# Optimization experiments

Measured on AMD Instinct MI355X. Metric: run time of the kernel, lower is better.

Reference implementation:

```python
import jax, jax.numpy as jnp
import numpy as np

T = 8192
INPUT = 1024
TRACE = 64
CTX = 16
OUT = 1024
EPS = 1e-5  # equinox LayerNorm default


def _linear(key, out_f, in_f):
    k1, k2 = jax.random.split(key)
    lim = 1.0 / np.sqrt(in_f)
    w = jax.random.uniform(k1, (out_f, in_f), minval=-lim, maxval=lim, dtype=jnp.float32)
    b = jax.random.uniform(k2, (out_f,), minval=-lim, maxval=lim, dtype=jnp.float32)
    return w, b


def setup_inputs() -> dict:
    key = jax.random.key(0)
    ks = jax.random.split(key, 8)
    x = jax.random.normal(ks[0], (T, INPUT), dtype=jnp.float32)
    start = jax.random.randint(ks[1], (T,), 0, 2).astype(bool)
    next_done = jax.random.randint(ks[2], (T,), 0, 2).astype(bool)
    state_re = jnp.zeros((1, TRACE, CTX), dtype=jnp.float32)
    state_im = jnp.zeros((1, TRACE, CTX), dtype=jnp.float32)
    pre_w, pre_b = _linear(ks[3], TRACE, INPUT)
    gi_w, gi_b = _linear(ks[4], TRACE, INPUT)
    go_w, go_b = _linear(ks[5], OUT, INPUT)
    skip_w, skip_b = _linear(ks[6], OUT, INPUT)
    mix_w, mix_b = _linear(ks[7], OUT, 2 * TRACE * CTX)
    # ffa.init: deterministic decay rates a and oscillation freqs b
    ffa_a = jnp.linspace(1e-6, 0.5, TRACE, dtype=jnp.float32)
    ffa_b = (2.0 * jnp.pi / jnp.exp(jnp.linspace(jnp.log(1.0), jnp.log(1024.0), CTX))).astype(jnp.float32)
    return dict(x=x, state_re=state_re, state_im=state_im, start=start, next_done=next_done,
                pre_w=pre_w, pre_b=pre_b, gi_w=gi_w, gi_b=gi_b, go_w=go_w, go_b=go_b,
                skip_w=skip_w, skip_b=skip_b, mix_w=mix_w, mix_b=mix_b,
                ffa_a=ffa_a, ffa_b=ffa_b)


def _ffa_apply(ffa_a, ffa_b, gated_x, state0, start):
    """Resettable complex linear recurrence: s_t = gamma * s_{t-1} + x_t, reset at episode starts.
    gamma = exp(-|a| + i b), outer over (trace, context). Parallelized with an associative scan
    over monoid elements (reset_flag, state, elapsed_steps)."""
    Tn, m = gated_x.shape
    c = ffa_b.shape[0]
    ab = jax.lax.complex(
        jnp.broadcast_to(-jnp.abs(ffa_a)[None, :, None], (1, m, c)),
        jnp.broadcast_to(ffa_b[None, None, :], (1, m, c)),
    )  # [1, m, c] complex: log-gamma per unit timestep

    xc = jnp.broadcast_to(gated_x[:, :, None].astype(jnp.complex64), (Tn, m, c))
    # prepend carried-in recurrent state: timestep 0, no reset
    x_e = jnp.concatenate([state0.astype(jnp.complex64), xc], axis=0)          # [T+1, m, c]
    s_e = jnp.concatenate([jnp.zeros((1, 1, 1), bool), start[:, None, None]], axis=0)
    i_e = jnp.concatenate([jnp.zeros((1, 1, 1), jnp.float32),
                           jnp.ones((Tn, 1, 1), jnp.float32)], axis=0)

    def op(a, b):
        s1, x1, i1 = a
        s2, x2, i2 = b
        # zero the carried state across episode boundaries
        x1 = jnp.where(s2, 0.0, x1)
        i1 = jnp.where(s2, 0.0, i1)
        g = jnp.exp(ab * i2.astype(jnp.complex64))  # decay over i2 elapsed steps
        return (jnp.logical_or(s1, s2), x1 * g + x2, i1 + i2)

    _, states, _ = jax.lax.associative_scan(op, (s_e, x_e, i_e), axis=0)
    return states[1:]  # [T, m, c] complex64


def reference(x, state_re, state_im, start, next_done,
              pre_w, pre_b, gi_w, gi_b, go_w, go_b,
              skip_w, skip_b, mix_w, mix_b, ffa_a, ffa_b):
    gate_in = jax.nn.sigmoid(x @ gi_w.T + gi_b)          # [T, trace]
    pre = x @ pre_w.T + pre_b                            # [T, trace]
    gated_x = pre * gate_in

    state0 = jax.lax.complex(state_re, state_im)         # [1, trace, ctx]
    state = _ffa_apply(ffa_a, ffa_b, gated_x, state0, start)  # [T, trace, ctx] complex

    z_in = jnp.concatenate([jnp.real(state), jnp.imag(state)], axis=-1)
    z_in = z_in.reshape(state.shape[0], -1)              # [T, 2*trace*ctx]
    z = z_in @ mix_w.T + mix_b                           # [T, out]

    gate_out = jax.nn.sigmoid(x @ go_w.T + go_b)         # [T, out]
    skip = x @ skip_w.T + skip_b                         # [T, out]

    zg = z * gate_out
    mu = zg.mean(-1, keepdims=True)
    var = ((zg - mu) ** 2).mean(-1, keepdims=True)
    ln = (zg - mu) / jnp.sqrt(var + EPS)                 # LayerNorm, no affine

    out = ln + skip * (1.0 - gate_out)
    final_state = state[-1:]
    return out, final_state


if __name__ == "__main__":
    inp = setup_inputs()
    out, fs = jax.jit(reference)(**inp)
    print(out.shape, out.dtype, fs.shape, fs.dtype)
```

## Files before the change

### kernel.cpp

```cpp
#include <hip/hip_runtime.h>
#include <math.h>

#define T_DIM 8192
#define IN_DIM 1024
#define TRACE 64
#define CTX 16
#define OUT_DIM 1024
#define KMIX 2048

typedef __attribute__((ext_vector_type(8))) short bf16x8;
typedef __attribute__((ext_vector_type(4))) float f32x4;
typedef __attribute__((ext_vector_type(16))) float f32x16;

__device__ __forceinline__ unsigned short f2bf(float f) {
    unsigned int u = __float_as_uint(f);
    u = (u + 0x7FFFu + ((u >> 16) & 1u)) >> 16;
    return (unsigned short)u;
}
__device__ __forceinline__ float bf2f(unsigned short b) {
    return __uint_as_float(((unsigned int)b) << 16);
}

__device__ __forceinline__ void gl2lds16(const void* g, void* l) {
    __builtin_amdgcn_global_load_lds(
        (const __attribute__((address_space(1))) unsigned int*)g,
        (__attribute__((address_space(3))) unsigned int*)l,
        16, 0, 0);
}


__global__ __launch_bounds__(256) void c0_conv(const float* __restrict__ x,
        const float* __restrict__ gw, const float* __restrict__ sw, const float* __restrict__ mw,
        const float* __restrict__ pw, const float* __restrict__ giw,
        const void* __restrict__ startp,
        unsigned short* __restrict__ xb, unsigned short* __restrict__ gob,
        unsigned short* __restrict__ skb, unsigned short* __restrict__ mixb,
        unsigned short* __restrict__ pwb, unsigned short* __restrict__ gwb,
        unsigned char* __restrict__ mask, unsigned long long* __restrict__ mask64)
{
    if (blockIdx.x == 0) {
        __shared__ int nonbool;
        int tid = threadIdx.x;
        if (tid == 0) nonbool = 0;
        __syncthreads();
        const unsigned int* wv = (const unsigned int*)startp;
        #pragma unroll
        for (int p = 0; p < 8; p++) {
            unsigned int a = wv[tid * 8 + p];
            if (a > 1u) nonbool = 1;
        }
        __syncthreads();
        if (nonbool) {
            const unsigned char* s8 = (const unsigned char*)startp;
            for (int i = tid; i < T_DIM; i += 256) mask[i] = (unsigned char)(s8[i] != 0);
        } else {
            const int* s32 = (const int*)startp;
            for (int i = tid; i < T_DIM; i += 256) mask[i] = (unsigned char)(s32[i] != 0);
        }
        __syncthreads();
        if (tid < 128) {
            unsigned long long wv2 = 0ull;
            int base = tid * 64;
            #pragma unroll 8
            for (int b2 = 0; b2 < 64; b2++)
                wv2 |= ((unsigned long long)(mask[base + b2] & 1)) << b2;
            mask64[tid] = wv2;
        }
    }
    const size_t QX = 2097152, QG = 262144, QS = 262144, QP = 16384, QI = 16384;
    const size_t totalA = QX + QG + QS + QP + QI;
    for (size_t q = (size_t)blockIdx.x * blockDim.x + threadIdx.x; q < totalA;
         q += (size_t)gridDim.x * blockDim.x) {
        const float* src; unsigned short* dst; size_t i;
        if (q < QX)               { src = x;   dst = xb;   i = q; }
        else if (q < QX+QG)       { src = gw;  dst = gob;  i = q - QX; }
        else if (q < QX+QG+QS)    { src = sw;  dst = skb;  i = q - QX - QG; }
        else if (q < QX+QG+QS+QP) { src = pw;  dst = pwb;  i = q - QX - QG - QS; }
        else                      { src = giw; dst = gwb;  i = q - QX - QG - QS - QP; }
        float4 v = *(const float4*)(src + i * 4);
        ushort4 o;
        o.x = f2bf(v.x); o.y = f2bf(v.y); o.z = f2bf(v.z); o.w = f2bf(v.w);
        *(ushort4*)(dst + i * 4) = o;
    }
    const size_t QM = 524288;
    for (size_t q = (size_t)blockIdx.x * blockDim.x + threadIdx.x; q < QM;
         q += (size_t)gridDim.x * blockDim.x) {
        float4 v = *(const float4*)(mw + q * 4);
        int flat = (int)(q * 4);
        int n  = flat >> 11;
        int kk = flat & 2047;
        int mm = kk >> 5;
        int w_ = kk & 31;
        int p  = w_ >> 4;
        int cc = w_ & 15;
        int kb = (n << 11) + mm * 32 + (cc << 1) + p;
        mixb[kb]     = f2bf(v.x);
        mixb[kb + 2] = f2bf(v.y);
        mixb[kb + 4] = f2bf(v.z);
        mixb[kb + 6] = f2bf(v.w);
    }
}

__global__ __launch_bounds__(256) void k1_mfma(const unsigned short* __restrict__ xb,
        const unsigned short* __restrict__ pwb, const unsigned short* __restrict__ gwb,
        const float* __restrict__ pre_b, const float* __restrict__ gi_b,
        float* __restrict__ gxT)
{
    __shared__ __align__(16) unsigned short As[1024];
    __shared__ __align__(16) unsigned short Bs[4096];
    __shared__ float sgE[64][33];

    const int tid = threadIdx.x;
    const int t0 = blockIdx.x * 32;
    const int lane = tid & 63, w = tid >> 6;
    const int quad = lane >> 4, l16 = lane & 15;
    const int r = tid >> 2, s4 = tid & 3;
    const int csw = (s4 - ((r >> 1) & 3)) & 3;

    f32x4 acc[2][2];
    const f32x4 zero4 = {0.f, 0.f, 0.f, 0.f};
    #pragma unroll
    for (int mi = 0; mi < 2; mi++)
        #pragma unroll
        for (int ni = 0; ni < 2; ni++) acc[mi][ni] = zero4;

    const int sfr = (quad + ((l16 >> 1) & 3)) & 3;

    for (int k0 = 0; k0 < IN_DIM; k0 += 32) {
        __syncthreads();
        if (tid < 128) {
            int ra = tid >> 2;
            int ca = ((tid & 3) - ((ra >> 1) & 3)) & 3;
            gl2lds16(xb + (size_t)(t0 + ra) * IN_DIM + k0 + ca * 8, As + tid * 8);
        }
        gl2lds16(pwb + (size_t)r * IN_DIM + k0 + csw * 8, Bs + tid * 8);
        gl2lds16(gwb + (size_t)r * IN_DIM + k0 + csw * 8, Bs + 2048 + tid * 8);
        asm volatile("s_waitcnt vmcnt(0)" ::: "memory");
        __syncthreads();
        bf16x8 af[2], bf[2];
        #pragma unroll
        for (int mi = 0; mi < 2; mi++)
            af[mi] = *(const bf16x8*)&As[(mi * 16 + l16) * 32 + sfr * 8];
        #pragma unroll
        for (int ni = 0; ni < 2; ni++)
            bf[ni] = *(const bf16x8*)&Bs[(w * 32 + ni * 16 + l16) * 32 + sfr * 8];
        #pragma unroll
        for (int mi = 0; mi < 2; mi++)
            #pragma unroll
            for (int ni = 0; ni < 2; ni++)
                acc[mi][ni] = __builtin_amdgcn_mfma_f32_16x16x32_bf16(af[mi], bf[ni], acc[mi][ni], 0, 0, 0);
    }

    if (w >= 2) {
        #pragma unroll
        for (int mi = 0; mi < 2; mi++)
            #pragma unroll
            for (int ni = 0; ni < 2; ni++) {
                int mg = (w - 2) * 32 + ni * 16 + l16;
                float gb = gi_b[mg];
                #pragma unroll
                for (int rr = 0; rr < 4; rr++) {
                    int tl = mi * 16 + quad * 4 + rr;
                    sgE[mg][tl] = 1.f / (1.f + expf(-(acc[mi][ni][rr] + gb)));
                }
            }
    }
    __syncthreads();
    if (w < 2) {
        #pragma unroll
        for (int mi = 0; mi < 2; mi++)
            #pragma unroll
            for (int ni = 0; ni < 2; ni++) {
                int mp = w * 32 + ni * 16 + l16;
                float pb = pre_b[mp];
                float4 o;
                float* po = &o.x;
                #pragma unroll
                for (int rr = 0; rr < 4; rr++) {
                    int tl = mi * 16 + quad * 4 + rr;
                    po[rr] = (acc[mi][ni][rr] + pb) * sgE[mp][tl];
                }
                *(float4*)&gxT[(size_t)mp * T_DIM + t0 + mi * 16 + quad * 4] = o;
            }
    }
}

__global__ __launch_bounds__(1024, 1) void k2_scan(const float* __restrict__ gxT,
        const unsigned long long* __restrict__ mask64,
        const float* __restrict__ state_re, const float* __restrict__ state_im,
        const float* __restrict__ ffa_a, const float* __restrict__ ffa_b,
        unsigned short* __restrict__ zinb, float* __restrict__ fstate)
{
    const int m = blockIdx.x;
    const int tid = threadIdx.x;
    const int c = tid & 15, j = tid >> 4;
    __shared__ __align__(16) float gxs[8192 + 128];
    __shared__ float Br[16][65], Bi[16][65], Er[16][65], Ei[16][65];
    __shared__ unsigned char Rf[16][65];

    const float am = -fabsf(ffa_a[m]);
    const float bc = ffa_b[c];
    const float er = expf(am);
    const float gr = er * cosf(bc);
    const float gi = er * sinf(bc);

    {
        const float4* gx4 = (const float4*)(gxT + (size_t)m * T_DIM);
        #pragma unroll
        for (int it = 0; it < 2; it++) {
            int g = it * 1024 + tid;
            float4 v = gx4[g];
            int t = g * 4;
            gxs[t     + ( t      >> 6)] = v.x;
            gxs[t + 1 + ((t + 1) >> 6)] = v.y;
            gxs[t + 2 + ((t + 2) >> 6)] = v.z;
            gxs[t + 3 + ((t + 3) >> 6)] = v.w;
        }
    }
    const unsigned long long mw0 = mask64[j * 2];
    const unsigned long long mw1 = mask64[j * 2 + 1];
    __syncthreads();

    const int lb = j * 130;
    float sre = 0.f, sim = 0.f;
    #pragma unroll 8
    for (int i = 0; i < 64; i++) {
        if ((mw0 >> i) & 1ull) { sre = 0.f; sim = 0.f; }
        else { float tr_ = sre * gr - sim * gi; sim = sre * gi + sim * gr; sre = tr_; }
        sre += gxs[lb + i];
    }
    #pragma unroll 8
    for (int i = 0; i < 64; i++) {
        if ((mw1 >> i) & 1ull) { sre = 0.f; sim = 0.f; }
        else { float tr_ = sre * gr - sim * gi; sim = sre * gi + sim * gr; sre = tr_; }
        sre += gxs[lb + 65 + i];
    }
    Br[c][j] = sre; Bi[c][j] = sim; Rf[c][j] = ((mw0 | mw1) != 0ull) ? 1 : 0;
    __syncthreads();

    if (tid < 16) {
        const int cc = tid;
        float b2 = 128.f * ffa_b[cc];
        float e128 = expf(128.f * am);
        float gRr = e128 * cosf(b2);
        float gRi = e128 * sinf(b2);
        float pr = state_re[m * CTX + cc], pi = state_im[m * CTX + cc];
        for (int q2 = 0; q2 < 64; q2++) {
            Er[cc][q2] = pr; Ei[cc][q2] = pi;
            if (Rf[cc][q2]) { pr = Br[cc][q2]; pi = Bi[cc][q2]; }
            else {
                float nr = pr * gRr - pi * gRi + Br[cc][q2];
                pi       = pr * gRi + pi * gRr + Bi[cc][q2];
                pr = nr;
            }
        }
    }
    __syncthreads();

    sre = Er[c][j]; sim = Ei[c][j];
    unsigned int* zout = (unsigned int*)zinb;
    const int obase = m * CTX + c;
    {
        const int tbase = j * 128;
        #pragma unroll 8
        for (int i = 0; i < 64; i++) {
            if ((mw0 >> i) & 1ull) { sre = 0.f; sim = 0.f; }
            else { float tr_ = sre * gr - sim * gi; sim = sre * gi + sim * gr; sre = tr_; }
            sre += gxs[lb + i];
            unsigned int u = (unsigned int)f2bf(sre) | ((unsigned int)f2bf(sim) << 16);
            zout[((size_t)(tbase + i) << 10) + obase] = u;
        }
        #pragma unroll 8
        for (int i = 0; i < 64; i++) {
            if ((mw1 >> i) & 1ull) { sre = 0.f; sim = 0.f; }
            else { float tr_ = sre * gr - sim * gi; sim = sre * gi + sim * gr; sre = tr_; }
            sre += gxs[lb + 65 + i];
            unsigned int u = (unsigned int)f2bf(sre) | ((unsigned int)f2bf(sim) << 16);
            zout[((size_t)(tbase + 64 + i) << 10) + obase] = u;
        }
    }
    if (j == 63) {
        fstate[obase]        = sre;
        fstate[1024 + obase] = sim;
    }
}

__global__ __launch_bounds__(512, 2) void gA_gemm(
        const unsigned short* __restrict__ xb,   const unsigned short* __restrict__ zinb,
        const unsigned short* __restrict__ gob,  const unsigned short* __restrict__ skb,
        const unsigned short* __restrict__ mixb,
        const float* __restrict__ go_b, const float* __restrict__ skip_b, const float* __restrict__ mix_b,
        unsigned short* __restrict__ zg, unsigned short* __restrict__ sk2)
{
    __shared__ __align__(16) unsigned short L[49152];
    const int tid = threadIdx.x;
    const int b = blockIdx.x;
    const int xcd = b & 7, q = b >> 3;
    const int t0 = (xcd * 4 + (q >> 3)) * 256;
    const int n0 = (q & 7) * 128;

    const int lane = tid & 63, w = tid >> 6;
    const int wm = w >> 1, wn = w & 1;
    const int l31 = lane & 31, h = lane >> 5;
    const int r = tid >> 2;
    const int csw = ((tid & 3) - ((r >> 1) & 3)) & 3;
    const int c8 = csw * 8;
    const int srot = (l31 >> 1) & 3;
    const int dst8 = tid * 8;

    f32x16 accg[2][2], acck[2][2];
    #pragma unroll
    for (int mi = 0; mi < 2; mi++)
        #pragma unroll
        for (int ni = 0; ni < 2; ni++)
            #pragma unroll
            for (int e = 0; e < 16; e++) { accg[mi][ni][e] = 0.f; acck[mi][ni][e] = 0.f; }

    {
        const unsigned short* gA0 = xb  + (size_t)(t0 + r)       * IN_DIM + c8;
        const unsigned short* gA1 = xb  + (size_t)(t0 + 128 + r) * IN_DIM + c8;
        const unsigned short* gB0 = gob + (size_t)(n0 + r)       * IN_DIM + c8;
        const unsigned short* gC0 = skb + (size_t)(n0 + r)       * IN_DIM + c8;

#define STAGE_F(bufi, kof) do {                         \
        unsigned short* _b = &L[(bufi) * 16384];        \
        gl2lds16(gA0 + (kof), _b + dst8);               \
        gl2lds16(gA1 + (kof), _b + 4096 + dst8);        \
        gl2lds16(gB0 + (kof), _b + 8192 + dst8);        \
        gl2lds16(gC0 + (kof), _b + 12288 + dst8);       \
    } while (0)

#define STEP_F(T, CUR, NXT, DOST, VMC) do {             \
        const unsigned short* As = &L[(CUR) * 16384];   \
        const unsigned short* Bs = As + 8192;           \
        const unsigned short* Cs = As + 12288;          \
        _Pragma("unroll")                               \
        for (int kh = 0; kh < 2; kh++) {                \
            const int so = ((kh * 2 + h + srot) & 3) * 8; \
            bf16x8 af[2], bg[2], bk[2];                 \
            _Pragma("unroll")                           \
            for (int mi = 0; mi < 2; mi++)              \
                af[mi] = *(const bf16x8*)&As[(wm * 64 + mi * 32 + l31) * 32 + so]; \
            _Pragma("unroll")                           \
            for (int ni = 0; ni < 2; ni++) {            \
                bg[ni] = *(const bf16x8*)&Bs[(wn * 64 + ni * 32 + l31) * 32 + so]; \
                bk[ni] = *(const bf16x8*)&Cs[(wn * 64 + ni * 32 + l31) * 32 + so]; \
            }                                           \
            if (kh == 0 && (DOST)) STAGE_F(NXT, ((T) + 2) * 32); \
            __builtin_amdgcn_s_setprio(1);              \
            _Pragma("unroll")                           \
            for (int mi = 0; mi < 2; mi++)              \
                _Pragma("unroll")                       \
                for (int ni = 0; ni < 2; ni++) {        \
                    accg[mi][ni] = __builtin_amdgcn_mfma_f32_32x32x16_bf16(af[mi], bg[ni], accg[mi][ni], 0, 0, 0); \
                    acck[mi][ni] = __builtin_amdgcn_mfma_f32_32x32x16_bf16(af[mi], bk[ni], acck[mi][ni], 0, 0, 0); \
                }                                       \
            __builtin_amdgcn_s_setprio(0);              \
        }                                               \
        asm volatile("s_waitcnt vmcnt(" #VMC ")" ::: "memory"); \
        __builtin_amdgcn_s_barrier();                   \
    } while (0)

        STAGE_F(0, 0);
        STAGE_F(1, 32);
        asm volatile("s_waitcnt vmcnt(4)" ::: "memory");
        __builtin_amdgcn_s_barrier();

        for (int t3i = 0; t3i < 30; t3i += 3) {
            STEP_F(t3i,     0, 2, 1, 4);
            STEP_F(t3i + 1, 1, 0, 1, 4);
            STEP_F(t3i + 2, 2, 1, 1, 4);
        }
        STEP_F(30, 0, 2, 0, 0);
        STEP_F(31, 1, 0, 0, 0);
#undef STEP_F
#undef STAGE_F
    }

    unsigned int sigp[32];
    #pragma unroll
    for (int mi = 0; mi < 2; mi++)
        #pragma unroll
        for (int ni = 0; ni < 2; ni++) {
            int n = n0 + wn * 64 + ni * 32 + l31;
            float gb = go_b[n];
            float sb_ = skip_b[n];
            #pragma unroll
            for (int reg = 0; reg < 16; reg++) {
                int row = (reg & 3) + 8 * (reg >> 2) + 4 * h;
                int t = t0 + wm * 64 + mi * 32 + row;
                float s = 1.f / (1.f + expf(-(accg[mi][ni][reg] + gb)));
                sk2[(size_t)t * OUT_DIM + n] = f2bf((acck[mi][ni][reg] + sb_) * (1.f - s));
                unsigned int pk = (unsigned int)f2bf(s);
                int idx = (mi * 2 + ni) * 8 + (reg >> 1);
                if (reg & 1) sigp[idx] |= pk << 16;
                else         sigp[idx]  = pk;
            }
        }

    #pragma unroll
    for (int mi = 0; mi < 2; mi++)
        #pragma unroll
        for (int ni = 0; ni < 2; ni++)
            #pragma unroll
            for (int e = 0; e < 16; e++) accg[mi][ni][e] = 0.f;
    {
        const unsigned short* mA0 = zinb + (size_t)(t0 + r)       * KMIX + c8;
        const unsigned short* mA1 = zinb + (size_t)(t0 + 128 + r) * KMIX + c8;
        const unsigned short* mB0 = mixb + (size_t)(n0 + r)       * KMIX + c8;

#define STAGE_M(bufi, kof) do {                         \
        unsigned short* _b = &L[(bufi) * 16384];        \
        gl2lds16(mA0 + (kof), _b + dst8);               \
        gl2lds16(mA1 + (kof), _b + 4096 + dst8);        \
        gl2lds16(mB0 + (kof), _b + 8192 + dst8);        \
    } while (0)

#define STEP_M(T, CUR, NXT, DOST, VMC) do {             \
        const unsigned short* As = &L[(CUR) * 16384];   \
        const unsigned short* Bs = As + 8192;           \
        _Pragma("unroll")                               \
        for (int kh = 0; kh < 2; kh++) {                \
            const int so = ((kh * 2 + h + srot) & 3) * 8; \
            bf16x8 af[2], bf[2];                        \
            _Pragma("unroll")                           \
            for (int mi = 0; mi < 2; mi++)              \
                af[mi] = *(const bf16x8*)&As[(wm * 64 + mi * 32 + l31) * 32 + so]; \
            _Pragma("unroll")                           \
            for (int ni = 0; ni < 2; ni++)              \
                bf[ni] = *(const bf16x8*)&Bs[(wn * 64 + ni * 32 + l31) * 32 + so]; \
            if (kh == 0 && (DOST)) STAGE_M(NXT, ((T) + 2) * 32); \
            __builtin_amdgcn_s_setprio(1);              \
            _Pragma("unroll")                           \
            for (int mi = 0; mi < 2; mi++)              \
                _Pragma("unroll")                       \
                for (int ni = 0; ni < 2; ni++)          \
                    accg[mi][ni] = __builtin_amdgcn_mfma_f32_32x32x16_bf16(af[mi], bf[ni], accg[mi][ni], 0, 0, 0); \
            __builtin_amdgcn_s_setprio(0);              \
        }                                               \
        asm volatile("s_waitcnt vmcnt(" #VMC ")" ::: "memory"); \
        __builtin_amdgcn_s_barrier();                   \
    } while (0)

        STAGE_M(0, 0);
        STAGE_M(1, 32);
        asm volatile("s_waitcnt vmcnt(3)" ::: "memory");
        __builtin_amdgcn_s_barrier();

        for (int t3i = 0; t3i < 60; t3i += 3) {
            STEP_M(t3i,     0, 2, 1, 3);
            STEP_M(t3i + 1, 1, 0, 1, 3);
            STEP_M(t3i + 2, 2, 1, 1, 3);
        }
        STEP_M(60, 0, 2, 1, 3);
        STEP_M(61, 1, 0, 1, 3);
        STEP_M(62, 2, 1, 0, 0);
        STEP_M(63, 0, 2, 0, 0);
#undef STEP_M
#undef STAGE_M
    }

    #pragma unroll
    for (int mi = 0; mi < 2; mi++)
        #pragma unroll
        for (int ni = 0; ni < 2; ni++) {
            int n = n0 + wn * 64 + ni * 32 + l31;
            float mb_ = mix_b[n];
            #pragma unroll
            for (int reg = 0; reg < 16; reg++) {
                int row = (reg & 3) + 8 * (reg >> 2) + 4 * h;
                int t = t0 + wm * 64 + mi * 32 + row;
                unsigned int u = sigp[(mi * 2 + ni) * 8 + (reg >> 1)];
                float sig = bf2f((unsigned short)((reg & 1) ? (u >> 16) : (u & 0xffff)));
                zg[(size_t)t * OUT_DIM + n] = f2bf((accg[mi][ni][reg] + mb_) * sig);
            }
        }
}

__global__ __launch_bounds__(256) void g3_ln(const unsigned short* __restrict__ zg,
        const unsigned short* __restrict__ sk2, const float* __restrict__ fstate,
        float* __restrict__ out, int out_size)
{
    __shared__ float sb[4], qb[4];
    __shared__ float mu_s, rstd_s;
    const int t = blockIdx.x;
    const int tid = threadIdx.x;
    ushort4 zu = *(const ushort4*)&zg [(size_t)t * OUT_DIM + tid * 4];
    ushort4 su = *(const ushort4*)&sk2[(size_t)t * OUT_DIM + tid * 4];
    float z0 = bf2f(zu.x), z1 = bf2f(zu.y), z2 = bf2f(zu.z), z3 = bf2f(zu.w);
    float s0 = bf2f(su.x), s1 = bf2f(su.y), s2 = bf2f(su.z), s3 = bf2f(su.w);
    float s = z0 + z1 + z2 + z3;
    float q = z0*z0 + z1*z1 + z2*z2 + z3*z3;
    #pragma unroll
    for (int off = 32; off > 0; off >>= 1) {
        s += __shfl_down(s, off, 64);
        q += __shfl_down(q, off, 64);
    }
    int wid = tid >> 6;
    if ((tid & 63) == 0) { sb[wid] = s; qb[wid] = q; }
    __syncthreads();
    if (tid == 0) {
        float S = sb[0] + sb[1] + sb[2] + sb[3];
        float Q = qb[0] + qb[1] + qb[2] + qb[3];
        float mu = S * (1.f / 1024.f);
        float var = Q * (1.f / 1024.f) - mu * mu;
        mu_s = mu; rstd_s = rsqrtf(var + 1e-5f);
    }
    __syncthreads();
    float mu = mu_s, rs = rstd_s;
    float4 o;
    o.x = (z0 - mu) * rs + s0;
    o.y = (z1 - mu) * rs + s1;
    o.z = (z2 - mu) * rs + s2;
    o.w = (z3 - mu) * rs + s3;
    *(float4*)&out[(size_t)t * OUT_DIM + tid * 4] = o;

    if (t < 8) {
        int i = t * 256 + tid;
        long long base = (long long)T_DIM * OUT_DIM;
        if (base + i < (long long)out_size) out[base + i] = fstate[i];
    }
}

extern "C" void kernel_launch(void* const* d_in, const int* in_sizes, int n_in,
                              void* d_out, int out_size, void* d_ws, size_t ws_size,
                              hipStream_t stream) {
    const float* x        = (const float*)d_in[0];
    const float* state_re = (const float*)d_in[1];
    const float* state_im = (const float*)d_in[2];
    const void*  startp   = d_in[3];
    const float* pre_w    = (const float*)d_in[5];
    const float* pre_b    = (const float*)d_in[6];
    const float* gi_w     = (const float*)d_in[7];
    const float* gi_b     = (const float*)d_in[8];
    const float* go_w     = (const float*)d_in[9];
    const float* go_b     = (const float*)d_in[10];
    const float* skip_w   = (const float*)d_in[11];
    const float* skip_b   = (const float*)d_in[12];
    const float* mix_w    = (const float*)d_in[13];
    const float* mix_b    = (const float*)d_in[14];
    const float* ffa_a    = (const float*)d_in[15];
    const float* ffa_b    = (const float*)d_in[16];

    float* ws = (float*)d_ws;
    float*          gxT    = ws;
    unsigned short* zinb   = (unsigned short*)(ws + 8912896);
    unsigned short* xb     = (unsigned short*)(ws + 17301504);
    unsigned short* gob    = (unsigned short*)(ws + 21495808);
    unsigned short* skb    = (unsigned short*)(ws + 22020096);
    unsigned short* mixb   = (unsigned short*)(ws + 22544384);
    unsigned short* zg     = (unsigned short*)(ws + 23592960);
    unsigned short* sk2    = (unsigned short*)(ws + 27787264);
    float*          fstate = ws + 31981568;
    unsigned char*  mask   = (unsigned char*)(ws + 31983616);
    unsigned long long* mask64 = (unsigned long long*)(ws + 31985664);
    unsigned short* pwb    = zg;
    unsigned short* gwb    = zg + 65536;
    float* out = (float*)d_out;

    hipLaunchKernelGGL(c0_conv,  dim3(1536), dim3(256),  0, stream, x, go_w, skip_w, mix_w, pre_w, gi_w,
                                                          startp, xb, gob, skb, mixb, pwb, gwb, mask, mask64);
    hipLaunchKernelGGL(k1_mfma,  dim3(256),  dim3(256),  0, stream, xb, pwb, gwb, pre_b, gi_b, gxT);
    hipLaunchKernelGGL(k2_scan,  dim3(64),   dim3(1024), 0, stream, gxT, mask64, state_re, state_im, ffa_a, ffa_b, zinb, fstate);
    hipLaunchKernelGGL(gA_gemm,  dim3(256),  dim3(512),  0, stream, xb, zinb, gob, skb, mixb, go_b, skip_b, mix_b, zg, sk2);
    hipLaunchKernelGGL(g3_ln,    dim3(8192), dim3(256),  0, stream, zg, sk2, fstate, out, out_size);
}
```

Before: 263.4 us.

## Split scan output phase across four blocks per trace unit

```diff
diff --git a/kernel.cpp b/kernel.cpp
--- a/kernel.cpp
+++ b/kernel.cpp
@@ -191,12 +191,15 @@
         const float* __restrict__ ffa_a, const float* __restrict__ ffa_b,
         unsigned short* __restrict__ zinb, float* __restrict__ fstate)
 {
-    const int m = blockIdx.x;
+    const int m  = blockIdx.x >> 2;
+    const int qd = blockIdx.x & 3;
     const int tid = threadIdx.x;
     const int c = tid & 15, j = tid >> 4;
     __shared__ __align__(16) float gxs[8192 + 128];
     __shared__ float Br[16][65], Bi[16][65], Er[16][65], Ei[16][65];
     __shared__ unsigned char Rf[16][65];
+    __shared__ float B32r[16][16][3], B32i[16][16][3];
+    __shared__ unsigned char sRf[16][16][3];
 
     const float am = -fabsf(ffa_a[m]);
     const float bc = ffa_b[c];
@@ -222,18 +225,39 @@
     __syncthreads();
 
     const int lb = j * 130;
+    const int gloc = j - qd * 16;
+    const bool own = (unsigned)gloc < 16u;
+
     float sre = 0.f, sim = 0.f;
     #pragma unroll 8
-    for (int i = 0; i < 64; i++) {
+    for (int i = 0; i < 32; i++) {
         if ((mw0 >> i) & 1ull) { sre = 0.f; sim = 0.f; }
         else { float tr_ = sre * gr - sim * gi; sim = sre * gi + sim * gr; sre = tr_; }
         sre += gxs[lb + i];
     }
+    if (own) { B32r[c][gloc][0] = sre; B32i[c][gloc][0] = sim;
+               sRf[c][gloc][0] = ((mw0 & 0xffffffffull) != 0ull) ? 1 : 0; }
     #pragma unroll 8
-    for (int i = 0; i < 64; i++) {
+    for (int i = 0; i < 32; i++) {
+        if ((mw0 >> (i + 32)) & 1ull) { sre = 0.f; sim = 0.f; }
+        else { float tr_ = sre * gr - sim * gi; sim = sre * gi + sim * gr; sre = tr_; }
+        sre += gxs[lb + 32 + i];
+    }
+    if (own) { B32r[c][gloc][1] = sre; B32i[c][gloc][1] = sim;
+               sRf[c][gloc][1] = (mw0 != 0ull) ? 1 : 0; }
+    #pragma unroll 8
+    for (int i = 0; i < 32; i++) {
         if ((mw1 >> i) & 1ull) { sre = 0.f; sim = 0.f; }
         else { float tr_ = sre * gr - sim * gi; sim = sre * gi + sim * gr; sre = tr_; }
         sre += gxs[lb + 65 + i];
+    }
+    if (own) { B32r[c][gloc][2] = sre; B32i[c][gloc][2] = sim;
+               sRf[c][gloc][2] = ((mw0 != 0ull) || ((mw1 & 0xffffffffull) != 0ull)) ? 1 : 0; }
+    #pragma unroll 8
+    for (int i = 0; i < 32; i++) {
+        if ((mw1 >> (i + 32)) & 1ull) { sre = 0.f; sim = 0.f; }
+        else { float tr_ = sre * gr - sim * gi; sim = sre * gi + sim * gr; sre = tr_; }
+        sre += gxs[lb + 97 + i];
     }
     Br[c][j] = sre; Bi[c][j] = sim; Rf[c][j] = ((mw0 | mw1) != 0ull) ? 1 : 0;
     __syncthreads();
@@ -257,31 +281,41 @@
     }
     __syncthreads();
 
-    sre = Er[c][j]; sim = Ei[c][j];
-    unsigned int* zout = (unsigned int*)zinb;
-    const int obase = m * CTX + c;
     {
-        const int tbase = j * 128;
+        const int gl2 = j >> 2, s = j & 3;
+        const int g = qd * 16 + gl2;
+        const unsigned long long w0 = mask64[g * 2];
+        const unsigned long long w1 = mask64[g * 2 + 1];
+        const unsigned int mbits = (unsigned int)(((s < 2) ? w0 : w1) >> ((s & 1) * 32));
+        float str, sti;
+        {
+            float E_r = Er[c][g], E_i = Ei[c][g];
+            if (s == 0) { str = E_r; sti = E_i; }
+            else if (sRf[c][gl2][s - 1]) { str = B32r[c][gl2][s - 1]; sti = B32i[c][gl2][s - 1]; }
+            else {
+                float ang = 32.f * (float)s * bc;
+                float mag = expf(32.f * (float)s * am);
+                float gsr = mag * cosf(ang), gsi = mag * sinf(ang);
+                str = B32r[c][gl2][s - 1] + E_r * gsr - E_i * gsi;
+                sti = B32i[c][gl2][s - 1] + E_r * gsi + E_i * gsr;
+            }
+        }
+        const int pb = g * 130 + (s >> 1) * 65 + (s & 1) * 32;
+        const int tstart = g * 128 + s * 32;
+        unsigned int* zout = (unsigned int*)zinb;
+        const int obase = m * CTX + c;
         #pragma unroll 8
-        for (int i = 0; i < 64; i++) {
-            if ((mw0 >> i) & 1ull) { sre = 0.f; sim = 0.f; }
-            else { float tr_ = sre * gr - sim * gi; sim = sre * gi + sim * gr; sre = tr_; }
-            sre += gxs[lb + i];
-            unsigned int u = (unsigned int)f2bf(sre) | ((unsigned int)f2bf(sim) << 16);
-            zout[((size_t)(tbase + i) << 10) + obase] = u;
-        }
-        #pragma unroll 8
-        for (int i = 0; i < 64; i++) {
-            if ((mw1 >> i) & 1ull) { sre = 0.f; sim = 0.f; }
-            else { float tr_ = sre * gr - sim * gi; sim = sre * gi + sim * gr; sre = tr_; }
-            sre += gxs[lb + 65 + i];
-            unsigned int u = (unsigned int)f2bf(sre) | ((unsigned int)f2bf(sim) << 16);
-            zout[((size_t)(tbase + 64 + i) << 10) + obase] = u;
-        }
-    }
-    if (j == 63) {
-        fstate[obase]        = sre;
-        fstate[1024 + obase] = sim;
+        for (int i = 0; i < 32; i++) {
+            if ((mbits >> i) & 1u) { str = 0.f; sti = 0.f; }
+            else { float tr_ = str * gr - sti * gi; sti = str * gi + sti * gr; str = tr_; }
+            str += gxs[pb + i];
+            unsigned int u = (unsigned int)f2bf(str) | ((unsigned int)f2bf(sti) << 16);
+            zout[((size_t)(tstart + i) << 10) + obase] = u;
+        }
+        if (qd == 3 && j == 63) {
+            fstate[obase]        = str;
+            fstate[1024 + obase] = sti;
+        }
     }
 }
 
@@ -561,7 +595,7 @@
     hipLaunchKernelGGL(c0_conv,  dim3(1536), dim3(256),  0, stream, x, go_w, skip_w, mix_w, pre_w, gi_w,
                                                           startp, xb, gob, skb, mixb, pwb, gwb, mask, mask64);
     hipLaunchKernelGGL(k1_mfma,  dim3(256),  dim3(256),  0, stream, xb, pwb, gwb, pre_b, gi_b, gxT);
-    hipLaunchKernelGGL(k2_scan,  dim3(64),   dim3(1024), 0, stream, gxT, mask64, state_re, state_im, ffa_a, ffa_b, zinb, fstate);
+    hipLaunchKernelGGL(k2_scan,  dim3(256),  dim3(1024), 0, stream, gxT, mask64, state_re, state_im, ffa_a, ffa_b, zinb, fstate);
     hipLaunchKernelGGL(gA_gemm,  dim3(256),  dim3(512),  0, stream, xb, zinb, gob, skb, mixb, go_b, skip_b, mix_b, zg, sk2);
     hipLaunchKernelGGL(g3_ln,    dim3(8192), dim3(256),  0, stream, zg, sk2, fstate, out, out_size);
 }
```

Result: faster. 257.0 us (-2.4%).
